# Performance work log

Hardware: AMD Instinct MI355X
Metric: run time of the kernel (lower is better)

The kernel has to match this reference:

```python
import jax, jax.numpy as jnp
import numpy as np

B, S, HID = 4, 4096, 1024
HEADS, D = 8, 128          # head_dim = HID // HEADS
NSEG, SEGLEN = 16, 256     # SEGLEN = S // NSEG
E, I = 16, 512             # num_experts, intermediate_size


def setup_inputs() -> dict:
    key = jax.random.key(0)
    ks = jax.random.split(key, 8)
    return {
        "x": jax.random.normal(ks[0], (B, S, HID), jnp.float32),
        "W_mh": jax.random.normal(ks[1], (HID, HID), jnp.float32) * (1.0 / np.sqrt(HID)),
        "b_mh": jax.random.normal(ks[2], (HID,), jnp.float32) * 0.02,
        "W_merge": jax.random.normal(ks[3], (HID, HID), jnp.float32) * (1.0 / np.sqrt(HID)),
        "b_merge": jnp.zeros((HID,), jnp.float32),
        "expert_embeddings": jax.random.normal(ks[4], (D, E), jnp.float32) * (1.0 / np.sqrt(D)),
        "first_linear": jax.random.normal(ks[5], (E, I, D), jnp.float32) * (1.0 / np.sqrt(D)),
        "second_linear": jax.random.normal(ks[6], (E, D, I), jnp.float32) * (1.0 / np.sqrt(I)),
    }


def reference(x, W_mh, b_mh, W_merge, b_merge, expert_embeddings, first_linear, second_linear):
    # multi-head projection
    x = x @ W_mh.T + b_mh                                   # [B,S,HID]
    # split into segments/heads (faithful to torch reshape order)
    x = x.reshape(B, NSEG, SEGLEN, HEADS, D)                # [B,N,L,H,D]
    avg = jnp.mean(x, axis=2)                               # [B,N,H,D]
    # router: softmax over experts
    ew = jax.nn.softmax(jnp.einsum('bnhd,de->bnhe', avg, expert_embeddings), axis=-1)
    # merge expert weight matrices (equivalent to torch's broadcast-mul-sum)
    m1 = jnp.einsum('eid,bnhe->bnhid', first_linear, ew)    # [B,N,H,I,D]
    m2 = jnp.einsum('edi,bnhe->bnhdi', second_linear, ew)   # [B,N,H,D,I]
    # NOTE: torch uses reshape (not permute) here -> mixes seglen/head axes; replicate.
    xr = x.reshape(B, NSEG, HEADS, SEGLEN, D)               # [B,N,H,L,D]
    # causal shift: segment s uses weights from segment s-1
    x_causal = xr[:, 1:]
    h = jax.nn.relu(jnp.einsum('bnhld,bnhid->bnhli', x_causal, m1[:, :-1]))
    res = jnp.einsum('bnhli,bnhdi->bnhld', h, m2[:, :-1])   # [B,N-1,H,L,D]
    # segment 0 special case (no_grad in torch -> stop_gradient)
    h0 = jax.nn.relu(jnp.einsum('bhld,bhid->bhli', xr[:, 0], m1[:, 0]))
    r0 = jnp.einsum('bhli,bhdi->bhld', h0, m2[:, 0])
    r0 = jax.lax.stop_gradient(r0)[:, None]                 # [B,1,H,L,D]
    out = jnp.concatenate([r0, res], axis=1)                # [B,N,H,L,D]
    out = out.reshape(B, S, HEADS, D).reshape(B, S, HID)
    return out @ W_merge.T + b_merge
```

## Files before the change

kernel.cpp:

```cpp
#include <hip/hip_runtime.h>
#include <hip/hip_bf16.h>

typedef _Float16 f16;
typedef f16 f16x2 __attribute__((ext_vector_type(2)));
typedef f16 f16x4 __attribute__((ext_vector_type(4)));
typedef f16 f16x8 __attribute__((ext_vector_type(8)));
typedef float f32x2 __attribute__((ext_vector_type(2)));
typedef float f32x4 __attribute__((ext_vector_type(4)));

#define MFMA16(a, b, c) __builtin_amdgcn_mfma_f32_16x16x32_f16(a, b, c, 0, 0, 0)

__device__ __forceinline__ void glds16(const void* g, void* l) {
    __builtin_amdgcn_global_load_lds(
        (const __attribute__((address_space(1))) unsigned int*)g,
        (__attribute__((address_space(3))) unsigned int*)l, 16, 0, 0);
}

#define VM8 asm volatile("s_waitcnt vmcnt(8)" ::: "memory")
#define VM6 asm volatile("s_waitcnt vmcnt(6)" ::: "memory")
#define VM4 asm volatile("s_waitcnt vmcnt(4)" ::: "memory")
#define VM0 asm volatile("s_waitcnt vmcnt(0)" ::: "memory")
#define VMN do {} while (0)
#define SB0 __builtin_amdgcn_sched_barrier(0)

__global__ __launch_bounds__(256) void cvt_kernel(const float* __restrict__ s,
                                                  f16* __restrict__ d, int n) {
    int i = (blockIdx.x * 256 + threadIdx.x) * 8;
    if (i >= n) return;
    float4 a = *(const float4*)(s + i);
    float4 b = *(const float4*)(s + i + 4);
    f16x8 h;
    h[0] = (f16)a.x; h[1] = (f16)a.y; h[2] = (f16)a.z; h[3] = (f16)a.w;
    h[4] = (f16)b.x; h[5] = (f16)b.y; h[6] = (f16)b.z; h[7] = (f16)b.w;
    *(f16x8*)(d + i) = h;
}

template <int MH, int NH, bool LOADA>
__device__ __forceinline__ void phase_rw(const f16* Aslab, const f16* Bslab,
                                         f16x8 (&af)[4][2], f16x8 (&bf)[2][2],
                                         int cl, int q, int wm, int wn) {
    if (LOADA) {
#pragma unroll
        for (int mt = 0; mt < 4; ++mt)
#pragma unroll
            for (int ks = 0; ks < 2; ++ks)
                af[mt][ks] =
                    *(const f16x8*)&Aslab[(wm * 64 + mt * 16 + cl) * 64 +
                                          ((ks * 4 + q) ^ (cl & 7)) * 8];
    }
#pragma unroll
    for (int nt = 0; nt < 2; ++nt)
#pragma unroll
        for (int ks = 0; ks < 2; ++ks)
            bf[nt][ks] = *(const f16x8*)&Bslab[(wn * 32 + nt * 16 + cl) * 64 +
                                               ((ks * 4 + q) ^ (cl & 7)) * 8];
}

template <int MH, int NH>
__device__ __forceinline__ void phase_mm(f16x8 (&af)[4][2], f16x8 (&bf)[2][2],
                                         f32x4 (&acc)[8][4]) {
    __builtin_amdgcn_s_setprio(1);
#pragma unroll
    for (int mt = 0; mt < 4; ++mt)
#pragma unroll
        for (int nt = 0; nt < 2; ++nt)
#pragma unroll
            for (int ks = 0; ks < 2; ++ks)
                acc[MH * 4 + mt][NH * 2 + nt] =
                    MFMA16(af[mt][ks], bf[nt][ks], acc[MH * 4 + mt][NH * 2 + nt]);
    __builtin_amdgcn_s_setprio(0);
}

__device__ __forceinline__ void stage_half(const f16* gsrc, int ldk, f16* ldst,
                                           int w, int lane) {
#pragma unroll
    for (int j = 0; j < 2; ++j) {
        int idx = j * 512 + w * 64 + lane;
        int rr = idx >> 3;
        int gs = (idx & 7) ^ (rr & 7);
        glds16(gsrc + (size_t)rr * ldk + gs * 8, ldst + (j * 512 + w * 64) * 8);
    }
}

#define SA(DB, H, KT) stage_half(A16 + (size_t)(mb * 256 + (H)*128) * K + (KT)*64, \
                                 K, Ad[DB][H], w, lane)
#define SBm(DB, H, KT) stage_half(Bw + (size_t)(nb * 256 + (H)*128) * K + (KT)*64, \
                                  K, Bd[DB][H], w, lane)

#define PH(DB, MH, NH, LA, STAGE, VMC)                                    \
    phase_rw<MH, NH, LA>(Ad[DB][MH], Bd[DB][NH], af, bf, cl, q, wm, wn);  \
    STAGE;                                                                \
    SB0; __builtin_amdgcn_s_barrier(); SB0;                               \
    phase_mm<MH, NH>(af, bf, acc);                                        \
    VMC;                                                                  \
    SB0; __builtin_amdgcn_s_barrier(); SB0;

template <bool OUT_F16>
__global__ __launch_bounds__(512, 2) void gemm256_kernel(
    const f16* __restrict__ A16, const f16* __restrict__ Bw,
    const float* __restrict__ bias, void* __restrict__ C_, int M, int N, int K) {
    __shared__ f16 Ad[2][2][128 * 64];
    __shared__ f16 Bd[2][2][128 * 64];
    const int tid = threadIdx.x;
    const int lane = tid & 63;
    const int w = tid >> 6;
    const int wm = w >> 2, wn = w & 3;
    const int q = lane >> 4, cl = lane & 15;
    const int nblk = N >> 8;
    const int cpx = (int)gridDim.x >> 3;
    const int logical = ((int)blockIdx.x & 7) * cpx + ((int)blockIdx.x >> 3);
    const int mb = logical / nblk, nb = logical % nblk;

    f32x4 acc[8][4] = {};
    f16x8 af[4][2], bf[2][2];
    const int ITERS = (K >> 6) / 2;

    SA(0, 0, 0); SBm(0, 0, 0); SBm(0, 1, 0); SA(0, 1, 0);
    SA(1, 0, 1); SBm(1, 0, 1);
    VM8;
    SB0; __builtin_amdgcn_s_barrier(); SB0;

#pragma unroll 1
    for (int i = 0; i < ITERS - 1; ++i) {
        const int k2 = 2 * i;
        PH(0, 0, 0, true,  SA(1, 1, k2 + 1),  VM8)
        PH(0, 0, 1, false, SBm(1, 1, k2 + 1), VM8)
        PH(0, 1, 0, true,  SA(0, 0, k2 + 2),  VMN)
        PH(0, 1, 1, false, SBm(0, 0, k2 + 2), VM8)
        PH(1, 0, 0, true,  SBm(0, 1, k2 + 2), VM6)
        PH(1, 0, 1, false, SA(0, 1, k2 + 2),  VMN)
        PH(1, 1, 0, true,  SA(1, 0, k2 + 3),  VMN)
        PH(1, 1, 1, false, SBm(1, 0, k2 + 3), VM8)
    }
    {
        const int kl = 2 * ITERS - 1;
        PH(0, 0, 0, true,  SA(1, 1, kl),  VM8)
        PH(0, 0, 1, false, SBm(1, 1, kl), VM8)
        PH(0, 1, 0, true,  VMN,           VMN)
        PH(0, 1, 1, false, VMN,           VM4)
        PH(1, 0, 0, true,  VMN,           VM0)
        PH(1, 0, 1, false, VMN,           VMN)
        PH(1, 1, 0, true,  VMN,           VMN)
        PH(1, 1, 1, false, VMN,           VMN)
    }

#pragma unroll
    for (int mt7 = 0; mt7 < 8; ++mt7) {
#pragma unroll
        for (int nt4 = 0; nt4 < 4; ++nt4) {
            int row0 = mb * 256 + (mt7 >> 2) * 128 + wm * 64 + (mt7 & 3) * 16 + q * 4;
            int col = nb * 256 + (nt4 >> 1) * 128 + wn * 32 + (nt4 & 1) * 16 + cl;
            float bv = bias[col];
#pragma unroll
            for (int r = 0; r < 4; ++r) {
                float v = acc[mt7][nt4][r] + bv;
                if (OUT_F16)
                    ((f16*)C_)[(size_t)(row0 + r) * N + col] = (f16)v;
                else
                    ((float*)C_)[(size_t)(row0 + r) * N + col] = v;
            }
        }
    }
}

__global__ __launch_bounds__(256) void avg_kernel(const f16* __restrict__ X1h,
                                                  float* __restrict__ partial) {
    const int bn = blockIdx.x >> 2, rc = blockIdx.x & 3;
    const int tid = threadIdx.x;
    const f16* base = X1h + (size_t)bn * 262144 + (size_t)rc * 65536 + tid * 4;
    float s0 = 0.f, s1 = 0.f, s2 = 0.f, s3 = 0.f;
    for (int l = 0; l < 64; ++l) {
        f16x4 v = *(const f16x4*)(base + (size_t)l * 1024);
        s0 += (float)v[0]; s1 += (float)v[1]; s2 += (float)v[2]; s3 += (float)v[3];
    }
    const float sc = 1.f / 256.f;
    float4 o = make_float4(s0 * sc, s1 * sc, s2 * sc, s3 * sc);
    *(float4*)(partial + (size_t)(bn * 4 + rc) * 1024 + tid * 4) = o;
}

__global__ __launch_bounds__(64) void router_kernel(const float* __restrict__ partial,
                                                    const float* __restrict__ emb,
                                                    float* __restrict__ ew) {
    const int t = blockIdx.x;
    const int bn = t >> 3, h = t & 7;
    const int lane = threadIdx.x;
    float acc = 0.f;
    const float* p = partial + (size_t)bn * 4096 + h * 128;
    if (lane < 16) {
        for (int d = 0; d < 128; ++d) {
            float a = p[d] + p[d + 1024] + p[d + 2048] + p[d + 3072];
            acc = fmaf(a, emb[d * 16 + lane], acc);
        }
    }
    float m = acc;
#pragma unroll
    for (int o = 8; o; o >>= 1) m = fmaxf(m, __shfl_xor(m, o));
    float pr = __expf(acc - m);
    float s = pr;
#pragma unroll
    for (int o = 8; o; o >>= 1) s += __shfl_xor(s, o);
    if (lane < 16) ew[t * 16 + lane] = pr / s;
}

__global__ __launch_bounds__(256) void mix_kernel(const float* __restrict__ ew,
                                                  const float* __restrict__ FL,
                                                  const float* __restrict__ SL,
                                                  f16* __restrict__ m1h,
                                                  f16* __restrict__ m2h) {
    const int bid = blockIdx.x;
    const int which = bid >> 10;
    const int tg = (bid >> 6) & 15;
    const int chunk = bid & 63;
    const float* src = which ? SL : FL;
    f16* dst = which ? m2h : m1h;
    const int tid = threadIdx.x;
    const int e0 = chunk * 1024 + tid * 4;

    f32x4 fl[16];
#pragma unroll
    for (int e = 0; e < 16; ++e)
        fl[e] = *(const f32x4*)(src + (size_t)e * 65536 + e0);

    const float* wbase = ew + (size_t)tg * 32 * 16;
    float wc[16];
#pragma unroll
    for (int e = 0; e < 16; ++e) wc[e] = wbase[e];

#pragma unroll 1
    for (int tt = 0; tt < 32; ++tt) {
        float wn2[16];
        if (tt < 31) {
#pragma unroll
            for (int e = 0; e < 16; ++e) wn2[e] = wbase[(tt + 1) * 16 + e];
        }
        f32x4 a = {0.f, 0.f, 0.f, 0.f};
#pragma unroll
        for (int e = 0; e < 16; ++e) {
            a[0] = fmaf(wc[e], fl[e][0], a[0]);
            a[1] = fmaf(wc[e], fl[e][1], a[1]);
            a[2] = fmaf(wc[e], fl[e][2], a[2]);
            a[3] = fmaf(wc[e], fl[e][3], a[3]);
        }
        f16x4 h;
        h[0] = (f16)a[0]; h[1] = (f16)a[1]; h[2] = (f16)a[2]; h[3] = (f16)a[3];
        *(f16x4*)(dst + (size_t)(tg * 32 + tt) * 65536 + e0) = h;
        if (tt < 31) {
#pragma unroll
            for (int e = 0; e < 16; ++e) wc[e] = wn2[e];
        }
    }
}

__device__ __forceinline__ void stage_m1(const f16* m1c, f16* dst, int w, int lane) {
#pragma unroll
    for (int j = 0; j < 4; ++j) {
        int idx = j * 256 + w * 64 + lane;
        int row = idx >> 4, g = idx & 15;
        glds16(m1c + (size_t)row * 128 + (g ^ (row & 7)) * 8,
               dst + (j * 256 + w * 64) * 8);
    }
}
__device__ __forceinline__ void stage_m2(const f16* m2c, f16* dst, int w, int lane) {
#pragma unroll
    for (int j = 0; j < 4; ++j) {
        int idx = j * 256 + w * 64 + lane;
        int row = idx >> 3, g = idx & 7;
        glds16(m2c + (size_t)row * 512 + (g ^ (row & 7)) * 8,
               dst + (j * 256 + w * 64) * 8);
    }
}

__global__ __launch_bounds__(256) void mlp_kernel(const f16* __restrict__ Xg,
                                                  const f16* __restrict__ m1h,
                                                  const f16* __restrict__ m2h,
                                                  f16* __restrict__ Yg) {
    __shared__ f16 W1[2][64 * 128];
    __shared__ f16 W2[2][128 * 64];
    __shared__ f16 Hs[128 * 64];
    const int cpx = (int)gridDim.x >> 3;
    const int logical = ((int)blockIdx.x & 7) * cpx + ((int)blockIdx.x >> 3);
    const int t = logical >> 1, lh = logical & 1;
    const int n = (t >> 3) & 15;
    const int tm = (n > 0) ? (t - 8) : t;
    const int tid = threadIdx.x;
    const int lane = tid & 63, w = tid >> 6;
    const int q = lane >> 4, cl = lane & 15;
    const int l0 = w * 32;

    const f16* Xsrc = Xg + (size_t)t * 32768 + lh * 16384;
    const f16* m1b = m1h + (size_t)tm * 65536;
    const f16* m2b = m2h + (size_t)tm * 65536;

    stage_m1(m1b, W1[0], w, lane);
    stage_m2(m2b, W2[0], w, lane);
    f16x8 xf[2][4];
#pragma unroll
    for (int lt = 0; lt < 2; ++lt) {
        int l = l0 + lt * 16 + cl;
#pragma unroll
        for (int ks = 0; ks < 4; ++ks)
            xf[lt][ks] = *(const f16x8*)(Xsrc + (size_t)l * 128 + ks * 32 + q * 8);
    }
    VM0;
    SB0; __builtin_amdgcn_s_barrier(); SB0;

    f32x4 acc2[2][8] = {};
#pragma unroll 1
    for (int ic = 0; ic < 8; ++ic) {
        const int pb = ic & 1, ob = pb ^ 1;
        if (ic < 7) stage_m1(m1b + (size_t)(ic + 1) * 8192, W1[ob], w, lane);
        SB0;
        __builtin_amdgcn_s_setprio(1);
#pragma unroll
        for (int it = 0; it < 4; ++it) {
            f16x8 af2[4];
#pragma unroll
            for (int ks = 0; ks < 4; ++ks) {
                int r = it * 16 + cl;
                af2[ks] = *(const f16x8*)&W1[pb][r * 128 +
                                                (((ks * 4 + q) ^ (r & 7))) * 8];
            }
            f32x4 a1[2] = {};
#pragma unroll
            for (int ks = 0; ks < 4; ++ks)
#pragma unroll
                for (int lt = 0; lt < 2; ++lt)
                    a1[lt] = MFMA16(af2[ks], xf[lt][ks], a1[lt]);
            int gi = 2 * it + (q >> 1);
            int sub = (q & 1) * 8;
#pragma unroll
            for (int lt = 0; lt < 2; ++lt) {
                int l = l0 + lt * 16 + cl;
                f16x4 hv;
                hv[0] = (f16)fmaxf(a1[lt][0], 0.f);
                hv[1] = (f16)fmaxf(a1[lt][1], 0.f);
                hv[2] = (f16)fmaxf(a1[lt][2], 0.f);
                hv[3] = (f16)fmaxf(a1[lt][3], 0.f);
                *(f16x4*)((char*)Hs + (size_t)l * 128 + ((gi ^ (l & 7)) << 4) + sub) =
                    hv;
            }
        }
        __builtin_amdgcn_s_setprio(0);
        if (ic < 7) { VM4; } else { VM0; }
        SB0; __builtin_amdgcn_s_barrier(); SB0;

        if (ic < 7) stage_m2(m2b + (ic + 1) * 64, W2[ob], w, lane);
        SB0;
        f16x8 hf[2][2];
#pragma unroll
        for (int lt = 0; lt < 2; ++lt)
#pragma unroll
            for (int ks = 0; ks < 2; ++ks) {
                int l = l0 + lt * 16 + cl;
                hf[lt][ks] =
                    *(const f16x8*)&Hs[l * 64 + (((ks * 4 + q) ^ (l & 7))) * 8];
            }
        __builtin_amdgcn_s_setprio(1);
#pragma unroll
        for (int nt = 0; nt < 8; ++nt) {
            f16x8 bf2[2];
#pragma unroll
            for (int ks = 0; ks < 2; ++ks) {
                int d = nt * 16 + cl;
                bf2[ks] = *(const f16x8*)&W2[pb][d * 64 +
                                                 (((ks * 4 + q) ^ (d & 7))) * 8];
            }
#pragma unroll
            for (int lt = 0; lt < 2; ++lt)
#pragma unroll
                for (int ks = 0; ks < 2; ++ks)
                    acc2[lt][nt] = MFMA16(hf[lt][ks], bf2[ks], acc2[lt][nt]);
        }
        __builtin_amdgcn_s_setprio(0);
        if (ic < 7) { VM4; }
        SB0; __builtin_amdgcn_s_barrier(); SB0;
    }

    f16* Yb = Yg + (size_t)t * 32768 + lh * 16384;
#pragma unroll
    for (int lt = 0; lt < 2; ++lt) {
#pragma unroll
        for (int nt = 0; nt < 8; ++nt) {
            int lr = l0 + lt * 16 + q * 4;
            int d = nt * 16 + cl;
#pragma unroll
            for (int r = 0; r < 4; ++r)
                Yb[(size_t)(lr + r) * 128 + d] = (f16)acc2[lt][nt][r];
        }
    }
}

extern "C" void kernel_launch(void* const* d_in, const int* in_sizes, int n_in,
                              void* d_out, int out_size, void* d_ws, size_t ws_size,
                              hipStream_t stream) {
    const float* x    = (const float*)d_in[0];
    const float* W_mh = (const float*)d_in[1];
    const float* b_mh = (const float*)d_in[2];
    const float* W_mg = (const float*)d_in[3];
    const float* b_mg = (const float*)d_in[4];
    const float* emb  = (const float*)d_in[5];
    const float* FL   = (const float*)d_in[6];
    const float* SL   = (const float*)d_in[7];

    char* ws = (char*)d_ws;
    f16*   X1h  = (f16*)(ws + 0);
    f16*   m1h  = (f16*)(ws + 33554432);
    f16*   X0h  = (f16*)(ws + 33554432);
    f16*   m2h  = (f16*)(ws + 100663296);
    f16*   Wmhh = (f16*)(ws + 167772160);
    f16*   Wmgh = (f16*)(ws + 169869312);
    float* part = (float*)(ws + 171966464);
    float* ew   = (float*)(ws + 173015040);

    cvt_kernel<<<512, 256, 0, stream>>>(W_mh, Wmhh, 1048576);
    cvt_kernel<<<512, 256, 0, stream>>>(W_mg, Wmgh, 1048576);
    cvt_kernel<<<8192, 256, 0, stream>>>(x, X0h, 16777216);
    gemm256_kernel<true><<<256, 512, 0, stream>>>(X0h, Wmhh, b_mh, X1h,
                                                  16384, 1024, 1024);
    avg_kernel<<<256, 256, 0, stream>>>(X1h, part);
    router_kernel<<<512, 64, 0, stream>>>(part, emb, ew);
    mix_kernel<<<2048, 256, 0, stream>>>(ew, FL, SL, m1h, m2h);
    mlp_kernel<<<1024, 256, 0, stream>>>(X1h, m1h, m2h, X1h);
    gemm256_kernel<false><<<256, 512, 0, stream>>>(X1h, Wmgh, b_mg, d_out,
                                                   16384, 1024, 1024);
}
```

Measured before the change: 210.7 us.

## Merge MLP half-blocks into 512-thread blocks with triple-buffered weight staging

Each MLP workgroup now covers a full 256-row segment tile with 8 waves, where before two 256-thread blocks each took half. Every block therefore loads the merged expert weight chunks once, not twice. Staging moves from double to triple buffering with a prefetch distance of two chunks, and the vmcnt waits are adjusted to match. This raises LDS use (three W1/W2 buffers plus a larger H tile) and halves the grid, which may reduce occupancy and latency hiding.

```diff
diff --git a/kernel.cpp b/kernel.cpp
--- a/kernel.cpp
+++ b/kernel.cpp
@@ -19,6 +19,7 @@
 #define VM8 asm volatile("s_waitcnt vmcnt(8)" ::: "memory")
 #define VM6 asm volatile("s_waitcnt vmcnt(6)" ::: "memory")
 #define VM4 asm volatile("s_waitcnt vmcnt(4)" ::: "memory")
+#define VM2 asm volatile("s_waitcnt vmcnt(2)" ::: "memory")
 #define VM0 asm volatile("s_waitcnt vmcnt(0)" ::: "memory")
 #define VMN do {} while (0)
 #define SB0 __builtin_amdgcn_sched_barrier(0)
@@ -251,35 +252,34 @@
     }
 }
 
-__device__ __forceinline__ void stage_m1(const f16* m1c, f16* dst, int w, int lane) {
-#pragma unroll
-    for (int j = 0; j < 4; ++j) {
-        int idx = j * 256 + w * 64 + lane;
+__device__ __forceinline__ void stage_m1(const f16* m1c, f16* dst, int tid) {
+#pragma unroll
+    for (int j = 0; j < 2; ++j) {
+        int idx = j * 512 + tid;
         int row = idx >> 4, g = idx & 15;
         glds16(m1c + (size_t)row * 128 + (g ^ (row & 7)) * 8,
-               dst + (j * 256 + w * 64) * 8);
-    }
-}
-__device__ __forceinline__ void stage_m2(const f16* m2c, f16* dst, int w, int lane) {
-#pragma unroll
-    for (int j = 0; j < 4; ++j) {
-        int idx = j * 256 + w * 64 + lane;
+               dst + ((idx & ~63)) * 8);
+    }
+}
+__device__ __forceinline__ void stage_m2(const f16* m2c, f16* dst, int tid) {
+#pragma unroll
+    for (int j = 0; j < 2; ++j) {
+        int idx = j * 512 + tid;
         int row = idx >> 3, g = idx & 7;
         glds16(m2c + (size_t)row * 512 + (g ^ (row & 7)) * 8,
-               dst + (j * 256 + w * 64) * 8);
-    }
-}
-
-__global__ __launch_bounds__(256) void mlp_kernel(const f16* __restrict__ Xg,
+               dst + ((idx & ~63)) * 8);
+    }
+}
+
+__global__ __launch_bounds__(512) void mlp_kernel(const f16* __restrict__ Xg,
                                                   const f16* __restrict__ m1h,
                                                   const f16* __restrict__ m2h,
                                                   f16* __restrict__ Yg) {
-    __shared__ f16 W1[2][64 * 128];
-    __shared__ f16 W2[2][128 * 64];
-    __shared__ f16 Hs[128 * 64];
+    __shared__ f16 W1[3][64 * 128];
+    __shared__ f16 W2[3][128 * 64];
+    __shared__ f16 Hs[256 * 64];
     const int cpx = (int)gridDim.x >> 3;
-    const int logical = ((int)blockIdx.x & 7) * cpx + ((int)blockIdx.x >> 3);
-    const int t = logical >> 1, lh = logical & 1;
+    const int t = ((int)blockIdx.x & 7) * cpx + ((int)blockIdx.x >> 3);
     const int n = (t >> 3) & 15;
     const int tm = (n > 0) ? (t - 8) : t;
     const int tid = threadIdx.x;
@@ -287,12 +287,14 @@
     const int q = lane >> 4, cl = lane & 15;
     const int l0 = w * 32;
 
-    const f16* Xsrc = Xg + (size_t)t * 32768 + lh * 16384;
+    const f16* Xsrc = Xg + (size_t)t * 32768;
     const f16* m1b = m1h + (size_t)tm * 65536;
     const f16* m2b = m2h + (size_t)tm * 65536;
 
-    stage_m1(m1b, W1[0], w, lane);
-    stage_m2(m2b, W2[0], w, lane);
+    stage_m1(m1b, W1[0], tid);
+    stage_m2(m2b, W2[0], tid);
+    stage_m1(m1b + 8192, W1[1], tid);
+    stage_m2(m2b + 64, W2[1], tid);
     f16x8 xf[2][4];
 #pragma unroll
     for (int lt = 0; lt < 2; ++lt) {
@@ -307,8 +309,8 @@
     f32x4 acc2[2][8] = {};
 #pragma unroll 1
     for (int ic = 0; ic < 8; ++ic) {
-        const int pb = ic & 1, ob = pb ^ 1;
-        if (ic < 7) stage_m1(m1b + (size_t)(ic + 1) * 8192, W1[ob], w, lane);
+        const int pb = ic % 3;
+        if (ic < 6) stage_m1(m1b + (size_t)(ic + 2) * 8192, W1[(ic + 2) % 3], tid);
         SB0;
         __builtin_amdgcn_s_setprio(1);
 #pragma unroll
@@ -318,7 +320,7 @@
             for (int ks = 0; ks < 4; ++ks) {
                 int r = it * 16 + cl;
                 af2[ks] = *(const f16x8*)&W1[pb][r * 128 +
-                                                (((ks * 4 + q) ^ (r & 7))) * 8];
+                                                 (((ks * 4 + q) ^ (r & 7))) * 8];
             }
             f32x4 a1[2] = {};
 #pragma unroll
@@ -341,10 +343,10 @@
             }
         }
         __builtin_amdgcn_s_setprio(0);
-        if (ic < 7) { VM4; } else { VM0; }
+        if (ic <= 5) { VM6; } else if (ic == 6) { VM4; } else { VM0; }
         SB0; __builtin_amdgcn_s_barrier(); SB0;
 
-        if (ic < 7) stage_m2(m2b + (ic + 1) * 64, W2[ob], w, lane);
+        if (ic < 6) stage_m2(m2b + (ic + 2) * 64, W2[(ic + 2) % 3], tid);
         SB0;
         f16x8 hf[2][2];
 #pragma unroll
@@ -372,11 +374,11 @@
                     acc2[lt][nt] = MFMA16(hf[lt][ks], bf2[ks], acc2[lt][nt]);
         }
         __builtin_amdgcn_s_setprio(0);
-        if (ic < 7) { VM4; }
+        if (ic <= 5) { VM6; } else if (ic == 6) { VM2; }
         SB0; __builtin_amdgcn_s_barrier(); SB0;
     }
 
-    f16* Yb = Yg + (size_t)t * 32768 + lh * 16384;
+    f16* Yb = Yg + (size_t)t * 32768;
 #pragma unroll
     for (int lt = 0; lt < 2; ++lt) {
 #pragma unroll
@@ -420,7 +422,7 @@
     avg_kernel<<<256, 256, 0, stream>>>(X1h, part);
     router_kernel<<<512, 64, 0, stream>>>(part, emb, ew);
     mix_kernel<<<2048, 256, 0, stream>>>(ew, FL, SL, m1h, m2h);
-    mlp_kernel<<<1024, 256, 0, stream>>>(X1h, m1h, m2h, X1h);
+    mlp_kernel<<<512, 512, 0, stream>>>(X1h, m1h, m2h, X1h);
     gemm256_kernel<false><<<256, 512, 0, stream>>>(X1h, Wmgh, b_mg, d_out,
                                                    16384, 1024, 1024);
 }
```

Result: no change. 214.5 us (+1.8%).

## Replace double-buffered weight staging with single shared buffer and synchronous loads

Applied to the files above, without the earlier changes.

Removes the double-buffered W1/W2 LDS arrays and uses one shared weight buffer that is loaded synchronously between the two GEMM phases, guarded by __syncthreads. This shrinks LDS use from about 80KB to 32KB per block, which may allow more blocks per CU, but it drops the prefetch overlap of global-to-LDS loads with MFMA compute. The explicit waitcnt tuning and setprio hints are also removed.

```diff
diff --git a/kernel.cpp b/kernel.cpp
--- a/kernel.cpp
+++ b/kernel.cpp
@@ -251,22 +251,20 @@
     }
 }
 
-__device__ __forceinline__ void stage_m1(const f16* m1c, f16* dst, int w, int lane) {
+__device__ __forceinline__ void stage_m1c(const f16* m1c, f16* dst, int tid) {
 #pragma unroll
     for (int j = 0; j < 4; ++j) {
-        int idx = j * 256 + w * 64 + lane;
+        int idx = j * 256 + tid;
         int row = idx >> 4, g = idx & 15;
-        glds16(m1c + (size_t)row * 128 + (g ^ (row & 7)) * 8,
-               dst + (j * 256 + w * 64) * 8);
-    }
-}
-__device__ __forceinline__ void stage_m2(const f16* m2c, f16* dst, int w, int lane) {
+        glds16(m1c + (size_t)row * 128 + (g ^ (row & 7)) * 8, dst + (idx & ~63) * 8);
+    }
+}
+__device__ __forceinline__ void stage_m2c(const f16* m2c, f16* dst, int tid) {
 #pragma unroll
     for (int j = 0; j < 4; ++j) {
-        int idx = j * 256 + w * 64 + lane;
+        int idx = j * 256 + tid;
         int row = idx >> 3, g = idx & 7;
-        glds16(m2c + (size_t)row * 512 + (g ^ (row & 7)) * 8,
-               dst + (j * 256 + w * 64) * 8);
+        glds16(m2c + (size_t)row * 512 + (g ^ (row & 7)) * 8, dst + (idx & ~63) * 8);
     }
 }
 
@@ -274,8 +272,7 @@
                                                   const f16* __restrict__ m1h,
                                                   const f16* __restrict__ m2h,
                                                   f16* __restrict__ Yg) {
-    __shared__ f16 W1[2][64 * 128];
-    __shared__ f16 W2[2][128 * 64];
+    __shared__ f16 Ws[128 * 64];
     __shared__ f16 Hs[128 * 64];
     const int cpx = (int)gridDim.x >> 3;
     const int logical = ((int)blockIdx.x & 7) * cpx + ((int)blockIdx.x >> 3);
@@ -291,8 +288,7 @@
     const f16* m1b = m1h + (size_t)tm * 65536;
     const f16* m2b = m2h + (size_t)tm * 65536;
 
-    stage_m1(m1b, W1[0], w, lane);
-    stage_m2(m2b, W2[0], w, lane);
+    stage_m1c(m1b, Ws, tid);
     f16x8 xf[2][4];
 #pragma unroll
     for (int lt = 0; lt < 2; ++lt) {
@@ -301,24 +297,19 @@
         for (int ks = 0; ks < 4; ++ks)
             xf[lt][ks] = *(const f16x8*)(Xsrc + (size_t)l * 128 + ks * 32 + q * 8);
     }
-    VM0;
-    SB0; __builtin_amdgcn_s_barrier(); SB0;
+    __syncthreads();
 
     f32x4 acc2[2][8] = {};
 #pragma unroll 1
     for (int ic = 0; ic < 8; ++ic) {
-        const int pb = ic & 1, ob = pb ^ 1;
-        if (ic < 7) stage_m1(m1b + (size_t)(ic + 1) * 8192, W1[ob], w, lane);
-        SB0;
-        __builtin_amdgcn_s_setprio(1);
 #pragma unroll
         for (int it = 0; it < 4; ++it) {
             f16x8 af2[4];
 #pragma unroll
             for (int ks = 0; ks < 4; ++ks) {
                 int r = it * 16 + cl;
-                af2[ks] = *(const f16x8*)&W1[pb][r * 128 +
-                                                (((ks * 4 + q) ^ (r & 7))) * 8];
+                af2[ks] = *(const f16x8*)&Ws[r * 128 +
+                                             (((ks * 4 + q) ^ (r & 7))) * 8];
             }
             f32x4 a1[2] = {};
 #pragma unroll
@@ -340,12 +331,10 @@
                     hv;
             }
         }
-        __builtin_amdgcn_s_setprio(0);
-        if (ic < 7) { VM4; } else { VM0; }
-        SB0; __builtin_amdgcn_s_barrier(); SB0;
-
-        if (ic < 7) stage_m2(m2b + (ic + 1) * 64, W2[ob], w, lane);
-        SB0;
+        __syncthreads();
+        stage_m2c(m2b + ic * 64, Ws, tid);
+        __syncthreads();
+
         f16x8 hf[2][2];
 #pragma unroll
         for (int lt = 0; lt < 2; ++lt)
@@ -355,15 +344,14 @@
                 hf[lt][ks] =
                     *(const f16x8*)&Hs[l * 64 + (((ks * 4 + q) ^ (l & 7))) * 8];
             }
-        __builtin_amdgcn_s_setprio(1);
 #pragma unroll
         for (int nt = 0; nt < 8; ++nt) {
             f16x8 bf2[2];
 #pragma unroll
             for (int ks = 0; ks < 2; ++ks) {
                 int d = nt * 16 + cl;
-                bf2[ks] = *(const f16x8*)&W2[pb][d * 64 +
-                                                 (((ks * 4 + q) ^ (d & 7))) * 8];
+                bf2[ks] = *(const f16x8*)&Ws[d * 64 +
+                                             (((ks * 4 + q) ^ (d & 7))) * 8];
             }
 #pragma unroll
             for (int lt = 0; lt < 2; ++lt)
@@ -371,9 +359,11 @@
                 for (int ks = 0; ks < 2; ++ks)
                     acc2[lt][nt] = MFMA16(hf[lt][ks], bf2[ks], acc2[lt][nt]);
         }
-        __builtin_amdgcn_s_setprio(0);
-        if (ic < 7) { VM4; }
-        SB0; __builtin_amdgcn_s_barrier(); SB0;
+        __syncthreads();
+        if (ic < 7) {
+            stage_m1c(m1b + (size_t)(ic + 1) * 8192, Ws, tid);
+            __syncthreads();
+        }
     }
 
     f16* Yb = Yg + (size_t)t * 32768 + lh * 16384;
```

New measurement: 207.5 us. About the same (-1.5%).
